# Kernel tuning notes

Hardware: AMD Instinct MI355X
Metric: run time of the kernel (lower is better)

Reference implementation:

```python
import jax, jax.numpy as jnp
import numpy as np
from jax import lax

_W = 0.8           # DVTV chroma weight (init kwarg w)
_ALPHA = 0.02      # forward default alpha
_EPS = 1e-8
_SQ3 = 3.0 ** 0.5; _SQ2 = 2.0 ** 0.5; _SQ6 = 6.0 ** 0.5
# orthonormal color decorrelation (luminance + 2 chroma)
_CMAT = np.array([[1/_SQ3, 1/_SQ3, 1/_SQ3],
                  [1/_SQ2, -1/_SQ2, 0.0],
                  [1/_SQ6, 1/_SQ6, -2/_SQ6]], dtype=np.float32)


def conv_csc(a, B):
    # a: (mb,P,C,M,N), B: (P,C,k,k) -> (mb,C,M,N): x_c = sum_p a_pc (corr) B_pc, SAME pad
    mb, P, C, M, N = a.shape
    a2 = a.transpose(0, 2, 1, 3, 4).reshape(mb, C * P, M, N)
    W = B.transpose(1, 0, 2, 3)  # (C, P, k, k): out=C, in/group=P
    return lax.conv_general_dilated(a2, W, (1, 1), 'SAME',
        dimension_numbers=('NCHW', 'OIHW', 'NCHW'), feature_group_count=C)


def convT_csc(r, B):
    # adjoint of conv_csc: (mb,C,M,N) -> (mb,P,C,M,N) via flipped-kernel correlation
    P, C, k, _ = B.shape
    mb, _, M, N = r.shape
    W = jnp.flip(B, (-2, -1)).transpose(1, 0, 2, 3).reshape(C * P, 1, k, k)
    o = lax.conv_general_dilated(r, W, (1, 1), 'SAME',
        dimension_numbers=('NCHW', 'OIHW', 'NCHW'), feature_group_count=C)
    return o.reshape(mb, C, P, M, N).transpose(0, 2, 1, 3, 4)


def Cop(x):
    return jnp.einsum('dc,bcmn->bdmn', jnp.asarray(_CMAT), x)


def Ctop(x):
    return jnp.einsum('cd,bcmn->bdmn', jnp.asarray(_CMAT), x)


def Dop(x):
    # forward differences, zero at boundary: (mb,C,M,N) -> (mb,2,C,M,N)
    dv = jnp.pad(x[:, :, 1:, :] - x[:, :, :-1, :], ((0, 0), (0, 0), (0, 1), (0, 0)))
    dh = jnp.pad(x[:, :, :, 1:] - x[:, :, :, :-1], ((0, 0), (0, 0), (0, 0), (0, 1)))
    return jnp.stack([dv, dh], axis=1)


def Dtop(y):
    # adjoint of Dop: (mb,2,C,M,N) -> (mb,C,M,N)
    yv = y[:, 0].at[:, :, -1, :].set(0.0)
    yh = y[:, 1].at[:, :, :, -1].set(0.0)
    dv = jnp.pad(yv[:, :, :-1, :], ((0, 0), (0, 0), (1, 0), (0, 0))) - yv
    dh = jnp.pad(yh[:, :, :, :-1], ((0, 0), (0, 0), (0, 0), (1, 0))) - yh
    return dv + dh


def soft(x, t):
    return jnp.sign(x) * jnp.maximum(jnp.abs(x) - t, 0.0)


def prox_dvtv(v, t, w):
    # group soft-threshold: lum group over grad dims; chroma group over grad dims + chroma channels
    lum, ch = v[:, :, 0:1], v[:, :, 1:]
    nl = jnp.sqrt(jnp.sum(lum * lum, axis=1, keepdims=True))
    nc = jnp.sqrt(jnp.sum(ch * ch, axis=(1, 2), keepdims=True))
    sl = jnp.maximum(0.0, 1.0 - t / jnp.maximum(nl, 1e-12))
    sc = jnp.maximum(0.0, 1.0 - (t * w) / jnp.maximum(nc, 1e-12))
    return jnp.concatenate([lum * sl, ch * sc], axis=2)


def proj_l2ball(v, z, radius):
    d = v - z
    n = jnp.sqrt(jnp.sum(d * d, axis=(1, 2, 3), keepdims=True))
    return z + d * jnp.minimum(1.0, radius / jnp.maximum(n, 1e-12))


def setup_inputs() -> dict:
    key = jax.random.key(0)
    k0, k1, k2, k3 = jax.random.split(key, 4)
    mb, C, M, N = 4, 3, 192, 192
    P, ksz, K = 32, 7, 8
    z = jax.random.uniform(k0, (mb, C, M, N), dtype=jnp.float32)
    mask = (jax.random.uniform(k1, (mb, C, M, N)) < 0.5).astype(jnp.float32)
    a0 = 0.01 * jax.random.normal(k2, (mb, P, C, M, N), dtype=jnp.float32)
    B = 0.01 * jax.random.normal(k3, (P, C, ksz, ksz), dtype=jnp.float32)
    # operator norm of B (max singular value of the per-channel filter banks, via FFT)
    Bn = np.asarray(B)
    acc = 0.0
    for c in range(C):
        H = np.fft.fft2(Bn[:, c], s=(64, 64))
        acc += float(np.max(np.sum(np.abs(H) ** 2, axis=0)))
    op_norm = float(np.sqrt(acc))
    beta = (1.0 + op_norm) ** 2
    g1 = 2.0 / beta * 0.9
    g3 = (1.0 / (1.0 + 4 * 2 + _W * 4 * 2)) * (1.0 / g1 - beta / 2.0)
    lam = jnp.full((K,), 5e-4, dtype=jnp.float32)
    return {
        'z': z, 'mask': mask, 'a0': a0, 'B': B,
        'lam1': lam, 'lam2': lam,
        'gam1': jnp.full((K,), g1, dtype=jnp.float32),
        'gam2': jnp.full((K,), g1, dtype=jnp.float32),
        'gam3': jnp.full((K,), g3, dtype=jnp.float32),
    }


def reference(z, mask, a0, B, lam1, lam2, gam1, gam2, gam3):
    mb, C, M, N = z.shape
    K = gam1.shape[0]
    radius = _ALPHA * float(np.sqrt(C * M * N))
    x_bef = z
    a_bef = a0
    y1_bef = jnp.zeros((mb, 2, C, M, N), dtype=z.dtype)
    y2_bef = jnp.zeros((mb, C, M, N), dtype=z.dtype)
    x_aft = x_bef
    for k in range(K):
        r = x_bef - conv_csc(a_bef, B)                     # shared residual
        x = x_bef - gam1[k] * (r + Ctop(Dtop(y1_bef)) + mask * y2_bef)
        x_aft = jnp.clip(x, 0.0, 1.0)                      # ProxBoxConstraint
        a = a_bef + gam2[k] * convT_csc(r, B)
        a_aft = soft(a, gam2[k] * lam1[k])                 # ProxL1
        v = 2.0 * x_aft - x_bef
        y1 = y1_bef + gam3[k] * Dop(Cop(v))
        y1_aft = y1 - gam3[k] * prox_dvtv(y1 / (gam3[k] + _EPS), lam2[k] / (gam3[k] + _EPS), _W)
        y2 = y2_bef + gam3[k] * (mask * v)
        y2_aft = y2 - gam3[k] * proj_l2ball(y2 / (gam3[k] + _EPS), z, radius)
        x_bef, a_bef, y1_bef, y2_bef = x_aft, a_aft, y1_aft, y2_aft
    return x_aft
```

## Files before the change

### kernel.cpp

```cpp
#include <hip/hip_runtime.h>

#define MB 4
#define CC 3
#define MM 192
#define NN 192
#define PP 32
#define KITER 8
#define MN (MM*NN)
#define CMN (CC*MN)
#define IMG (MB*CMN)
#define ASZ (MB*PP*CMN)

#define PSPLIT 16
#define PCHUNK (PP/PSPLIT)

#define PSPLIT_A 4
#define PCHUNK_A (PP/PSPLIT_A)

#define S3 0.57735026918962576f
#define S2 0.70710678118654752f
#define S6 0.40824829046386302f
#define W_CH 0.8f
#define EPSV 1e-8f
#define RADIUS 6.6510751010644885f

#define TD 64
#define HALO 3
#define HROWS 70
#define HCB 18
#define HS2 76
#define NF4 (HROWS*HCB)

#define TDIM 32
#define HT 38
#define HS 40
#define HTT (HT*HT)

__device__ __forceinline__ float softf(float x, float t) {
    float m = fabsf(x) - t;
    return m > 0.f ? copysignf(m, x) : 0.f;
}

__global__ __launch_bounds__(256) void k_conv_part(
    const float* __restrict__ a, const float* __restrict__ Bw,
    float* __restrict__ part)
{
    const int bc = blockIdx.z % (MB*CC);
    const int s  = blockIdx.z / (MB*CC);
    const int b = bc / CC, c = bc % CC;
    const int m0 = blockIdx.y * TD, n0 = blockIdx.x * TD;
    __shared__ float sT[HROWS * HS2];
    const int tc = threadIdx.x & 15;
    const int tr = threadIdx.x >> 4;
    const int p0 = s * PCHUNK;
    const int row0 = threadIdx.x / HCB;
    const int cb0  = threadIdx.x - row0*HCB;

    float4 pf[5];
    {
        const float* ap = a + (size_t)((b*PP + p0)*CC + c) * MN;
        int row = row0, cb = cb0;
        #pragma unroll
        for (int j = 0; j < 5; ++j) {
            const int gm = m0 + row - HALO;
            const int gc = n0 + cb*4 - 4;
            float4 v = {0.f,0.f,0.f,0.f};
            if (row < HROWS && (unsigned)gm < MM && (unsigned)gc <= (NN-4))
                v = *(const float4*)&ap[gm*NN + gc];
            pf[j] = v;
            cb += 4; row += 14; if (cb >= HCB) { cb -= HCB; row += 1; }
        }
    }
    float acc[4][4];
    #pragma unroll
    for (int r = 0; r < 4; ++r)
        #pragma unroll
        for (int j = 0; j < 4; ++j) acc[r][j] = 0.f;

    #pragma unroll 1
    for (int pp = 0; pp < PCHUNK; ++pp) {
        __syncthreads();
        {
            int row = row0, cb = cb0;
            #pragma unroll
            for (int j = 0; j < 5; ++j) {
                if (row < HROWS) *(float4*)&sT[row*HS2 + cb*4] = pf[j];
                cb += 4; row += 14; if (cb >= HCB) { cb -= HCB; row += 1; }
            }
        }
        __syncthreads();
        if (pp + 1 < PCHUNK) {
            const float* ap = a + (size_t)((b*PP + p0 + pp + 1)*CC + c) * MN;
            int row = row0, cb = cb0;
            #pragma unroll
            for (int j = 0; j < 5; ++j) {
                const int gm = m0 + row - HALO;
                const int gc = n0 + cb*4 - 4;
                float4 v = {0.f,0.f,0.f,0.f};
                if (row < HROWS && (unsigned)gm < MM && (unsigned)gc <= (NN-4))
                    v = *(const float4*)&ap[gm*NN + gc];
                pf[j] = v;
                cb += 4; row += 14; if (cb >= HCB) { cb -= HCB; row += 1; }
            }
        }
        const float* bp = Bw + ((p0 + pp)*CC + c) * 49;
        #pragma unroll
        for (int ir = 0; ir < 10; ++ir) {
            const int base = (tr*4 + ir)*HS2 + tc*4;
            const float4 q0 = *(const float4*)&sT[base];
            const float4 q1 = *(const float4*)&sT[base + 4];
            const float4 q2 = *(const float4*)&sT[base + 8];
            const float fl[12] = {q0.x,q0.y,q0.z,q0.w,q1.x,q1.y,q1.z,q1.w,
                                  q2.x,q2.y,q2.z,q2.w};
            #pragma unroll
            for (int r = 0; r < 4; ++r) {
                const int du = ir - r;
                if (du >= 0 && du <= 6) {
                    #pragma unroll
                    for (int v = 0; v < 7; ++v) {
                        const float bv = bp[du*7 + v];
                        #pragma unroll
                        for (int j = 0; j < 4; ++j) acc[r][j] += fl[v+j+1] * bv;
                    }
                }
            }
        }
    }
    #pragma unroll
    for (int r = 0; r < 4; ++r) {
        const int idx = (b*CC + c)*MN + (m0 + tr*4 + r)*NN + n0 + tc*4;
        float4 o; o.x = acc[r][0]; o.y = acc[r][1]; o.z = acc[r][2]; o.w = acc[r][3];
        *(float4*)&part[(size_t)s*IMG + idx] = o;
    }
}

__global__ __launch_bounds__(256) void k_a_update(
    const float* __restrict__ a_in, const float* __restrict__ rr,
    const float* __restrict__ Bw, float* __restrict__ a_out,
    const float* __restrict__ gam2, const float* __restrict__ lam1, int k)
{
    const int bc = blockIdx.z % (MB*CC);
    const int s  = blockIdx.z / (MB*CC);
    const int b = bc / CC, c = bc % CC;
    const int m0 = blockIdx.y * TDIM, n0 = blockIdx.x * TDIM;
    const float g2  = gam2[k];
    const float thr = g2 * lam1[k];
    __shared__ float sT[HT * HS];
    const float* rp = rr + (b*CC + c)*MN;
    for (int i = threadIdx.x; i < HTT; i += 256) {
        const int im = i / HT, in = i - im*HT;
        const int gm = m0 + im - 3, gn = n0 + in - 3;
        float v = 0.f;
        if ((unsigned)gm < MM && (unsigned)gn < NN) v = rp[gm*NN + gn];
        sT[im*HS + in] = v;
    }
    __syncthreads();
    const int row = threadIdx.x >> 3;
    const int tg  = threadIdx.x & 7;
    const int gm = m0 + row;
    const int gn = n0 + tg*4;
    const int p0 = s * PCHUNK_A;
    #pragma unroll 1
    for (int pp = 0; pp < PCHUNK_A; ++pp) {
        const int p = p0 + pp;
        const float* bp = Bw + (p*CC + c) * 49;
        float acc[4] = {0.f, 0.f, 0.f, 0.f};
        #pragma unroll
        for (int u = 0; u < 7; ++u) {
            const int base = (row + 6 - u)*HS + tg*4;
            const float4 q0 = *(const float4*)&sT[base];
            const float4 q1 = *(const float4*)&sT[base + 4];
            const float2 q2 = *(const float2*)&sT[base + 8];
            const float rv[10] = {q0.x,q0.y,q0.z,q0.w,q1.x,q1.y,q1.z,q1.w,q2.x,q2.y};
            #pragma unroll
            for (int v = 0; v < 7; ++v) {
                const float bv = bp[u*7 + v];
                acc[0] += rv[6-v] * bv;
                acc[1] += rv[7-v] * bv;
                acc[2] += rv[8-v] * bv;
                acc[3] += rv[9-v] * bv;
            }
        }
        const size_t idx = (size_t)((b*PP + p)*CC + c)*MN + gm*NN + gn;
        const float4 av = *(const float4*)&a_in[idx];
        float4 o;
        o.x = softf(av.x + g2*acc[0], thr);
        o.y = softf(av.y + g2*acc[1], thr);
        o.z = softf(av.z + g2*acc[2], thr);
        o.w = softf(av.w + g2*acc[3], thr);
        *(float4*)&a_out[idx] = o;
    }
}

__global__ __launch_bounds__(256) void k_x_update(
    const float* __restrict__ xbef, const float* __restrict__ part,
    float* __restrict__ rb,
    const float* __restrict__ y1, float* __restrict__ y2,
    const float* __restrict__ mask, const float* __restrict__ z,
    const float* __restrict__ gam1, const float* __restrict__ gam3, int k,
    float* __restrict__ xaft, float* __restrict__ sums)
{
    const int i = blockIdx.x*256 + threadIdx.x;
    const int b = i / CMN;
    const int rem = i - b*CMN;
    const int c = rem / MN;
    const int mn = rem - c*MN;
    const int m = mn / NN, n = mn - m*NN;
    const float g1 = gam1[k];
    const float g3 = gam3[k];
    const float inv3 = 1.f / (g3 + EPSV);
    float g3p = 0.f, invp = 0.f, scale_prev = 0.f;
    if (k > 0) {
        g3p  = gam3[k-1];
        invp = 1.f / (g3p + EPSV);
        const float nrm = sqrtf(sums[(k-1)*64 + b*16]);
        scale_prev = fminf(1.f, RADIUS / fmaxf(nrm, 1e-12f));
    }
    float dt[3];
    #pragma unroll
    for (int e = 0; e < 3; ++e) {
        const float* yv = y1 + ((size_t)(b*2 + 0)*CC + e)*MN;
        const float* yh = y1 + ((size_t)(b*2 + 1)*CC + e)*MN;
        float dv = (m > 0 ? yv[mn - NN] : 0.f) - (m < MM-1 ? yv[mn] : 0.f);
        float dh = (n > 0 ? yh[mn - 1]  : 0.f) - (n < NN-1 ? yh[mn] : 0.f);
        dt[e] = dv + dh;
    }
    const float ct0 = S3*dt[0] + S2*dt[1] + S6*dt[2];
    const float ct1 = S3*dt[0] - S2*dt[1] + S6*dt[2];
    const float ct2 = S3*dt[0]            - 2.f*S6*dt[2];
    const float ctc = (c == 0) ? ct0 : (c == 1) ? ct1 : ct2;
    const bool last = (k == KITER-1);

    float conv = 0.f;
    #pragma unroll
    for (int ss = 0; ss < PSPLIT; ++ss) conv += part[(size_t)ss*IMG + i];
    const float xb = xbef[i];
    const float r = xb - conv;
    const float zi = z[i];
    const float mk = mask[i];
    float y2b = 0.f;
    if (k > 0) {
        const float yr = y2[i];
        const float d = yr*invp - zi;
        y2b = yr - g3p*(zi + d*scale_prev);
    }
    float x = xb - g1*(r + ctc + mk*y2b);
    x = fminf(fmaxf(x, 0.f), 1.f);
    xaft[i] = x;
    float dsq = 0.f;
    if (!last) {
        rb[i] = r;
        const float v  = 2.f*x - xb;
        const float yn = y2b + g3*(mk*v);
        y2[i] = yn;
        const float d2 = yn*inv3 - zi;
        dsq = d2*d2;
    }
    if (!last) {
        #pragma unroll
        for (int off = 32; off > 0; off >>= 1) dsq += __shfl_down(dsq, off, 64);
        __shared__ float red[4];
        if ((threadIdx.x & 63) == 0) red[threadIdx.x >> 6] = dsq;
        __syncthreads();
        if (threadIdx.x == 0) {
            const int bb = blockIdx.x / (CMN/256);
            atomicAdd(&sums[k*64 + bb*16], red[0] + red[1] + red[2] + red[3]);
        }
    }
}

__global__ __launch_bounds__(256) void k_y1_update(
    float* __restrict__ y1, const float* __restrict__ xaft,
    const float* __restrict__ xbef,
    const float* __restrict__ gam3, const float* __restrict__ lam2, int k)
{
    const int i = blockIdx.x*256 + threadIdx.x;
    if (i >= MB*MN) return;
    const int b = i / MN, mn = i - b*MN;
    const int m = mn / NN, n = mn - m*NN;
    const float g3  = gam3[k];
    const float inv = 1.f / (g3 + EPSV);
    const float t   = lam2[k] * inv;
    const bool hasD = (m < MM-1), hasR = (n < NN-1);
    float vc[3], vd[3], vr[3];
    #pragma unroll
    for (int c = 0; c < 3; ++c) {
        const int idx = (b*CC + c)*MN + mn;
        vc[c] = 2.f*xaft[idx] - xbef[idx];
        vd[c] = hasD ? (2.f*xaft[idx+NN] - xbef[idx+NN]) : 0.f;
        vr[c] = hasR ? (2.f*xaft[idx+1]  - xbef[idx+1])  : 0.f;
    }
    const float cc0 = S3*(vc[0]+vc[1]+vc[2]);
    const float cc1 = S2*(vc[0]-vc[1]);
    const float cc2 = S6*(vc[0]+vc[1]) - 2.f*S6*vc[2];
    const float cd0 = S3*(vd[0]+vd[1]+vd[2]);
    const float cd1 = S2*(vd[0]-vd[1]);
    const float cd2 = S6*(vd[0]+vd[1]) - 2.f*S6*vd[2];
    const float cr0 = S3*(vr[0]+vr[1]+vr[2]);
    const float cr1 = S2*(vr[0]-vr[1]);
    const float cr2 = S6*(vr[0]+vr[1]) - 2.f*S6*vr[2];
    const float dv[3] = { hasD ? cd0-cc0 : 0.f, hasD ? cd1-cc1 : 0.f, hasD ? cd2-cc2 : 0.f };
    const float dh[3] = { hasR ? cr0-cc0 : 0.f, hasR ? cr1-cc1 : 0.f, hasR ? cr2-cc2 : 0.f };
    float yn[2][3], vv[2][3];
    #pragma unroll
    for (int e = 0; e < 3; ++e) {
        const int i0 = ((b*2 + 0)*CC + e)*MN + mn;
        const int i1 = ((b*2 + 1)*CC + e)*MN + mn;
        yn[0][e] = y1[i0] + g3*dv[e];
        yn[1][e] = y1[i1] + g3*dh[e];
        vv[0][e] = yn[0][e]*inv;
        vv[1][e] = yn[1][e]*inv;
    }
    const float nl = sqrtf(vv[0][0]*vv[0][0] + vv[1][0]*vv[1][0]);
    const float sl = fmaxf(0.f, 1.f - t / fmaxf(nl, 1e-12f));
    const float nc = sqrtf(vv[0][1]*vv[0][1] + vv[0][2]*vv[0][2]
                         + vv[1][1]*vv[1][1] + vv[1][2]*vv[1][2]);
    const float sc = fmaxf(0.f, 1.f - t*W_CH / fmaxf(nc, 1e-12f));
    #pragma unroll
    for (int e = 0; e < 3; ++e) {
        const float se = (e == 0) ? sl : sc;
        const int i0 = ((b*2 + 0)*CC + e)*MN + mn;
        const int i1 = ((b*2 + 1)*CC + e)*MN + mn;
        y1[i0] = yn[0][e] - g3*(vv[0][e]*se);
        y1[i1] = yn[1][e] - g3*(vv[1][e]*se);
    }
}

extern "C" void kernel_launch(void* const* d_in, const int* in_sizes, int n_in,
                              void* d_out, int out_size, void* d_ws, size_t ws_size,
                              hipStream_t stream) {
    const float* z    = (const float*)d_in[0];
    const float* mask = (const float*)d_in[1];
    const float* a0   = (const float*)d_in[2];
    const float* Bw   = (const float*)d_in[3];
    const float* lam1 = (const float*)d_in[4];
    const float* lam2 = (const float*)d_in[5];
    const float* gam1 = (const float*)d_in[6];
    const float* gam2 = (const float*)d_in[7];
    const float* gam3 = (const float*)d_in[8];
    float* out = (float*)d_out;

    float* ws = (float*)d_ws;
    float* xA   = ws; ws += IMG;
    float* xB   = ws; ws += IMG;
    float* y1   = ws; ws += 2*IMG;
    float* y2   = ws; ws += IMG;
    float* rb   = ws; ws += IMG;
    float* part = ws; ws += PSPLIT*IMG;
    float* sums = ws; ws += KITER*64;
    const size_t base_need = (size_t)((6 + PSPLIT)*IMG + KITER*64) * sizeof(float);
    float* a_ws;
    if (ws_size >= base_need + (size_t)ASZ * sizeof(float)) {
        a_ws = ws;
    } else {
        a_ws = (float*)d_in[2];
    }

    hipMemsetAsync(y1, 0, sizeof(float)*2*IMG, stream);
    hipMemsetAsync(sums, 0, sizeof(float)*KITER*64, stream);

    dim3 gconv(NN/TD, MM/TD, MB*CC*PSPLIT);
    dim3 ga(NN/TDIM, MM/TDIM, MB*CC*PSPLIT_A);
    const int ew_blocks  = (MB*MN) / 256;
    const int img_blocks = IMG / 256;

    const float* xbef = z;
    float* xaft = xA;
    const float* acur = a0;
    for (int k = 0; k < KITER; ++k) {
        k_conv_part<<<gconv, 256, 0, stream>>>(acur, Bw, part);
        float* xt = (k == KITER-1) ? out : xaft;
        k_x_update<<<img_blocks, 256, 0, stream>>>(xbef, part, rb, y1, y2, mask, z,
                                                   gam1, gam3, k, xt, sums);
        if (k < KITER-1) {
            k_a_update<<<ga, 256, 0, stream>>>(acur, rb, Bw, a_ws, gam2, lam1, k);
            k_y1_update<<<ew_blocks, 256, 0, stream>>>(y1, xt, xbef, gam3, lam2, k);
            acur = a_ws;
            xbef = xt;
            xaft = (xt == xA) ? xB : xA;
        }
    }
    (void)in_sizes; (void)n_in; (void)out_size;
}
```

Before: 730.3 us.

## Fuse sparse-code update with next iteration's forward convolution via shared-memory tile

The a-update kernel now computes the updated, soft-thresholded coefficients over a 38x38 tile with a 3-pixel halo and keeps it in shared memory. It then applies the forward convolution for the next iteration directly from that tile and writes per-split partial sums. This removes the separate forward-convolution kernel for every iteration after the first, along with its full re-read of the large coefficient tensor. In exchange, the halo region's update is recomputed redundantly by neighbouring tiles, the partial-sum split count changes, and coefficients are ping-ponged through the caller's a0 input buffer, which is overwritten.

```diff
diff --git a/kernel.cpp b/kernel.cpp
--- a/kernel.cpp
+++ b/kernel.cpp
@@ -14,8 +14,8 @@
 #define PSPLIT 16
 #define PCHUNK (PP/PSPLIT)
 
-#define PSPLIT_A 4
-#define PCHUNK_A (PP/PSPLIT_A)
+#define PSPLIT_F 4
+#define PCHUNK_F (PP/PSPLIT_F)
 
 #define S3 0.57735026918962576f
 #define S2 0.70710678118654752f
@@ -29,12 +29,10 @@
 #define HROWS 70
 #define HCB 18
 #define HS2 76
-#define NF4 (HROWS*HCB)
 
 #define TDIM 32
-#define HT 38
-#define HS 40
-#define HTT (HT*HT)
+#define SRS 48
+#define SAS 40
 
 __device__ __forceinline__ float softf(float x, float t) {
     float m = fabsf(x) - t;
@@ -134,9 +132,10 @@
     }
 }
 
-__global__ __launch_bounds__(256) void k_a_update(
-    const float* __restrict__ a_in, const float* __restrict__ rr,
+__global__ __launch_bounds__(256) void k_aconv(
+    const float* __restrict__ a_in, const float* __restrict__ rb,
     const float* __restrict__ Bw, float* __restrict__ a_out,
+    float* __restrict__ part,
     const float* __restrict__ gam2, const float* __restrict__ lam1, int k)
 {
     const int bc = blockIdx.z % (MB*CC);
@@ -145,55 +144,101 @@
     const int m0 = blockIdx.y * TDIM, n0 = blockIdx.x * TDIM;
     const float g2  = gam2[k];
     const float thr = g2 * lam1[k];
-    __shared__ float sT[HT * HS];
-    const float* rp = rr + (b*CC + c)*MN;
-    for (int i = threadIdx.x; i < HTT; i += 256) {
-        const int im = i / HT, in = i - im*HT;
-        const int gm = m0 + im - 3, gn = n0 + in - 3;
-        float v = 0.f;
-        if ((unsigned)gm < MM && (unsigned)gn < NN) v = rp[gm*NN + gn];
-        sT[im*HS + in] = v;
+    __shared__ float sR[44 * SRS];
+    __shared__ float sA[38 * SAS];
+
+    {
+        const float* rp = rb + (size_t)(b*CC + c) * MN;
+        #pragma unroll
+        for (int pass = 0; pass < 3; ++pass) {
+            const int f = threadIdx.x + pass*256;
+            if (f < 44*12) {
+                const int rrow = f / 12, rcb = f - rrow*12;
+                const int grow = m0 + rrow - 6;
+                const int gc4  = n0 - 8 + rcb*4;
+                float4 v = {0.f,0.f,0.f,0.f};
+                if ((unsigned)grow < MM && (unsigned)gc4 <= (NN-4))
+                    v = *(const float4*)&rp[grow*NN + gc4];
+                *(float4*)&sR[rrow*SRS + rcb*4] = v;
+            }
+        }
     }
     __syncthreads();
+
     const int row = threadIdx.x >> 3;
     const int tg  = threadIdx.x & 7;
-    const int gm = m0 + row;
-    const int gn = n0 + tg*4;
-    const int p0 = s * PCHUNK_A;
+    const int p0 = s * PCHUNK_F;
+    float accc[4] = {0.f, 0.f, 0.f, 0.f};
+
     #pragma unroll 1
-    for (int pp = 0; pp < PCHUNK_A; ++pp) {
+    for (int pp = 0; pp < PCHUNK_F; ++pp) {
         const int p = p0 + pp;
+        const size_t pbase = (size_t)((b*PP + p)*CC + c) * MN;
         const float* bp = Bw + (p*CC + c) * 49;
-        float acc[4] = {0.f, 0.f, 0.f, 0.f};
+
+        #pragma unroll
+        for (int pass = 0; pass < 2; ++pass) {
+            const int t = threadIdx.x + pass*256;
+            if (t < 380) {
+                const int ar  = t / 10;
+                const int acb = t - ar*10;
+                float acc[4] = {0.f, 0.f, 0.f, 0.f};
+                #pragma unroll
+                for (int u = 0; u < 7; ++u) {
+                    const float* srow = &sR[(ar + 6 - u)*SRS + acb*4];
+                    const float4 q0 = *(const float4*)&srow[0];
+                    const float4 q1 = *(const float4*)&srow[4];
+                    const float4 q2 = *(const float4*)&srow[8];
+                    const float fl[12] = {q0.x,q0.y,q0.z,q0.w,q1.x,q1.y,q1.z,q1.w,
+                                          q2.x,q2.y,q2.z,q2.w};
+                    #pragma unroll
+                    for (int v = 0; v < 7; ++v) {
+                        const float bv = bp[u*7 + v];
+                        #pragma unroll
+                        for (int j = 0; j < 4; ++j) acc[j] += fl[7 - v + j] * bv;
+                    }
+                }
+                const int gma = m0 + ar - 3;
+                const int gc4 = n0 - 4 + acb*4;
+                const bool ok = ((unsigned)gma < MM) && ((unsigned)gc4 <= (NN-4));
+                float4 av = {0.f,0.f,0.f,0.f};
+                if (ok) av = *(const float4*)&a_in[pbase + gma*NN + gc4];
+                float4 an;
+                an.x = ok ? softf(av.x + g2*acc[0], thr) : 0.f;
+                an.y = ok ? softf(av.y + g2*acc[1], thr) : 0.f;
+                an.z = ok ? softf(av.z + g2*acc[2], thr) : 0.f;
+                an.w = ok ? softf(av.w + g2*acc[3], thr) : 0.f;
+                *(float4*)&sA[ar*SAS + acb*4] = an;
+                if (ar >= 3 && ar <= 34 && acb >= 1 && acb <= 8)
+                    *(float4*)&a_out[pbase + gma*NN + gc4] = an;
+            }
+        }
+        __syncthreads();
+
         #pragma unroll
         for (int u = 0; u < 7; ++u) {
-            const int base = (row + 6 - u)*HS + tg*4;
-            const float4 q0 = *(const float4*)&sT[base];
-            const float4 q1 = *(const float4*)&sT[base + 4];
-            const float2 q2 = *(const float2*)&sT[base + 8];
-            const float rv[10] = {q0.x,q0.y,q0.z,q0.w,q1.x,q1.y,q1.z,q1.w,q2.x,q2.y};
+            const float* srow = &sA[(row + u)*SAS + tg*4];
+            const float4 q0 = *(const float4*)&srow[0];
+            const float4 q1 = *(const float4*)&srow[4];
+            const float4 q2 = *(const float4*)&srow[8];
+            const float fl[12] = {q0.x,q0.y,q0.z,q0.w,q1.x,q1.y,q1.z,q1.w,
+                                  q2.x,q2.y,q2.z,q2.w};
             #pragma unroll
             for (int v = 0; v < 7; ++v) {
                 const float bv = bp[u*7 + v];
-                acc[0] += rv[6-v] * bv;
-                acc[1] += rv[7-v] * bv;
-                acc[2] += rv[8-v] * bv;
-                acc[3] += rv[9-v] * bv;
-            }
-        }
-        const size_t idx = (size_t)((b*PP + p)*CC + c)*MN + gm*NN + gn;
-        const float4 av = *(const float4*)&a_in[idx];
-        float4 o;
-        o.x = softf(av.x + g2*acc[0], thr);
-        o.y = softf(av.y + g2*acc[1], thr);
-        o.z = softf(av.z + g2*acc[2], thr);
-        o.w = softf(av.w + g2*acc[3], thr);
-        *(float4*)&a_out[idx] = o;
-    }
+                #pragma unroll
+                for (int j = 0; j < 4; ++j) accc[j] += fl[1 + v + j] * bv;
+            }
+        }
+        __syncthreads();
+    }
+    const int idx = (b*CC + c)*MN + (m0 + row)*NN + n0 + tg*4;
+    float4 o; o.x = accc[0]; o.y = accc[1]; o.z = accc[2]; o.w = accc[3];
+    *(float4*)&part[(size_t)s*IMG + idx] = o;
 }
 
 __global__ __launch_bounds__(256) void k_x_update(
-    const float* __restrict__ xbef, const float* __restrict__ part,
+    const float* __restrict__ xbef, const float* __restrict__ part, int nsplit,
     float* __restrict__ rb,
     const float* __restrict__ y1, float* __restrict__ y2,
     const float* __restrict__ mask, const float* __restrict__ z,
@@ -232,8 +277,8 @@
     const bool last = (k == KITER-1);
 
     float conv = 0.f;
-    #pragma unroll
-    for (int ss = 0; ss < PSPLIT; ++ss) conv += part[(size_t)ss*IMG + i];
+    #pragma unroll 4
+    for (int ss = 0; ss < nsplit; ++ss) conv += part[(size_t)ss*IMG + i];
     const float xb = xbef[i];
     const float r = xb - conv;
     const float zi = z[i];
@@ -331,7 +376,7 @@
                               hipStream_t stream) {
     const float* z    = (const float*)d_in[0];
     const float* mask = (const float*)d_in[1];
-    const float* a0   = (const float*)d_in[2];
+    float*       a0   = (float*)d_in[2];
     const float* Bw   = (const float*)d_in[3];
     const float* lam1 = (const float*)d_in[4];
     const float* lam2 = (const float*)d_in[5];
@@ -349,33 +394,38 @@
     float* part = ws; ws += PSPLIT*IMG;
     float* sums = ws; ws += KITER*64;
     const size_t base_need = (size_t)((6 + PSPLIT)*IMG + KITER*64) * sizeof(float);
-    float* a_ws;
+    float* aA;
     if (ws_size >= base_need + (size_t)ASZ * sizeof(float)) {
-        a_ws = ws;
+        aA = ws;
     } else {
-        a_ws = (float*)d_in[2];
-    }
+        aA = a0;
+    }
+    float* aB = a0;
 
     hipMemsetAsync(y1, 0, sizeof(float)*2*IMG, stream);
     hipMemsetAsync(sums, 0, sizeof(float)*KITER*64, stream);
 
     dim3 gconv(NN/TD, MM/TD, MB*CC*PSPLIT);
-    dim3 ga(NN/TDIM, MM/TDIM, MB*CC*PSPLIT_A);
+    dim3 gf(NN/TDIM, MM/TDIM, MB*CC*PSPLIT_F);
     const int ew_blocks  = (MB*MN) / 256;
     const int img_blocks = IMG / 256;
 
     const float* xbef = z;
     float* xaft = xA;
     const float* acur = a0;
+    float* anext = aA;
     for (int k = 0; k < KITER; ++k) {
-        k_conv_part<<<gconv, 256, 0, stream>>>(acur, Bw, part);
+        if (k == 0)
+            k_conv_part<<<gconv, 256, 0, stream>>>(acur, Bw, part);
         float* xt = (k == KITER-1) ? out : xaft;
-        k_x_update<<<img_blocks, 256, 0, stream>>>(xbef, part, rb, y1, y2, mask, z,
+        k_x_update<<<img_blocks, 256, 0, stream>>>(xbef, part, (k == 0) ? PSPLIT : PSPLIT_F,
+                                                   rb, y1, y2, mask, z,
                                                    gam1, gam3, k, xt, sums);
         if (k < KITER-1) {
-            k_a_update<<<ga, 256, 0, stream>>>(acur, rb, Bw, a_ws, gam2, lam1, k);
+            k_aconv<<<gf, 256, 0, stream>>>(acur, rb, Bw, anext, part, gam2, lam1, k);
             k_y1_update<<<ew_blocks, 256, 0, stream>>>(y1, xt, xbef, gam3, lam2, k);
-            acur = a_ws;
+            acur = anext;
+            anext = (anext == aA) ? aB : aA;
             xbef = xt;
             xaft = (xt == xA) ? xB : xA;
         }
```

Result: slower. 1.532 ms (+109.8%).

## Drop shared-memory staging in conv kernels and read halos directly from global

Applied to the files above, without the earlier changes.

Both convolution kernels stop staging halo tiles in LDS and instead load float4 rows straight from global memory, relying on L1/L2 for reuse. The forward conv drops to 3 output rows per thread, uses 48x64 tiles and halves the P-split, which shrinks the partial-sum buffer the x-update reduces. The adjoint conv flips its loop order to reuse each residual row across all filters in its chunk, keeping 8x4 accumulators. The cost is more redundant global/cache traffic for overlapping halos and higher register pressure in exchange for removing syncs and LDS round trips.

```diff
diff --git a/kernel.cpp b/kernel.cpp
--- a/kernel.cpp
+++ b/kernel.cpp
@@ -11,9 +11,8 @@
 #define IMG (MB*CMN)
 #define ASZ (MB*PP*CMN)
 
-#define PSPLIT 16
-#define PCHUNK (PP/PSPLIT)
-
+#define PSPLIT_C 8
+#define PCHUNK_C (PP/PSPLIT_C)
 #define PSPLIT_A 4
 #define PCHUNK_A (PP/PSPLIT_A)
 
@@ -24,101 +23,55 @@
 #define EPSV 1e-8f
 #define RADIUS 6.6510751010644885f
 
-#define TD 64
-#define HALO 3
-#define HROWS 70
-#define HCB 18
-#define HS2 76
-#define NF4 (HROWS*HCB)
-
+#define TCW 64
+#define TCH 48
 #define TDIM 32
-#define HT 38
-#define HS 40
-#define HTT (HT*HT)
 
 __device__ __forceinline__ float softf(float x, float t) {
     float m = fabsf(x) - t;
     return m > 0.f ? copysignf(m, x) : 0.f;
 }
 
-__global__ __launch_bounds__(256) void k_conv_part(
+__global__ __launch_bounds__(256) void k_conv(
     const float* __restrict__ a, const float* __restrict__ Bw,
     float* __restrict__ part)
 {
     const int bc = blockIdx.z % (MB*CC);
     const int s  = blockIdx.z / (MB*CC);
     const int b = bc / CC, c = bc % CC;
-    const int m0 = blockIdx.y * TD, n0 = blockIdx.x * TD;
-    __shared__ float sT[HROWS * HS2];
+    const int m0 = blockIdx.y * TCH, n0 = blockIdx.x * TCW;
     const int tc = threadIdx.x & 15;
     const int tr = threadIdx.x >> 4;
-    const int p0 = s * PCHUNK;
-    const int row0 = threadIdx.x / HCB;
-    const int cb0  = threadIdx.x - row0*HCB;
-
-    float4 pf[5];
-    {
-        const float* ap = a + (size_t)((b*PP + p0)*CC + c) * MN;
-        int row = row0, cb = cb0;
-        #pragma unroll
-        for (int j = 0; j < 5; ++j) {
-            const int gm = m0 + row - HALO;
-            const int gc = n0 + cb*4 - 4;
-            float4 v = {0.f,0.f,0.f,0.f};
-            if (row < HROWS && (unsigned)gm < MM && (unsigned)gc <= (NN-4))
-                v = *(const float4*)&ap[gm*NN + gc];
-            pf[j] = v;
-            cb += 4; row += 14; if (cb >= HCB) { cb -= HCB; row += 1; }
-        }
-    }
-    float acc[4][4];
-    #pragma unroll
-    for (int r = 0; r < 4; ++r)
-        #pragma unroll
-        for (int j = 0; j < 4; ++j) acc[r][j] = 0.f;
+    const int gc = n0 + tc*4 - 4;
+    const bool pc0 = (unsigned)gc       <= (NN-4);
+    const bool pc1 = (unsigned)(gc + 4) <= (NN-4);
+    const bool pc2 = (unsigned)(gc + 8) <= (NN-4);
+    const int rbase = m0 + tr*3 - 3;
+    const int p0 = s * PCHUNK_C;
+    float acc[3][4] = {{0.f}};
 
     #pragma unroll 1
-    for (int pp = 0; pp < PCHUNK; ++pp) {
-        __syncthreads();
-        {
-            int row = row0, cb = cb0;
-            #pragma unroll
-            for (int j = 0; j < 5; ++j) {
-                if (row < HROWS) *(float4*)&sT[row*HS2 + cb*4] = pf[j];
-                cb += 4; row += 14; if (cb >= HCB) { cb -= HCB; row += 1; }
-            }
-        }
-        __syncthreads();
-        if (pp + 1 < PCHUNK) {
-            const float* ap = a + (size_t)((b*PP + p0 + pp + 1)*CC + c) * MN;
-            int row = row0, cb = cb0;
-            #pragma unroll
-            for (int j = 0; j < 5; ++j) {
-                const int gm = m0 + row - HALO;
-                const int gc = n0 + cb*4 - 4;
-                float4 v = {0.f,0.f,0.f,0.f};
-                if (row < HROWS && (unsigned)gm < MM && (unsigned)gc <= (NN-4))
-                    v = *(const float4*)&ap[gm*NN + gc];
-                pf[j] = v;
-                cb += 4; row += 14; if (cb >= HCB) { cb -= HCB; row += 1; }
-            }
-        }
+    for (int pp = 0; pp < PCHUNK_C; ++pp) {
+        const float* ap = a + (size_t)((b*PP + p0 + pp)*CC + c) * MN;
         const float* bp = Bw + ((p0 + pp)*CC + c) * 49;
         #pragma unroll
-        for (int ir = 0; ir < 10; ++ir) {
-            const int base = (tr*4 + ir)*HS2 + tc*4;
-            const float4 q0 = *(const float4*)&sT[base];
-            const float4 q1 = *(const float4*)&sT[base + 4];
-            const float4 q2 = *(const float4*)&sT[base + 8];
+        for (int u = 0; u < 9; ++u) {
+            const int gm = rbase + u;
+            const bool pr = (unsigned)gm < MM;
+            const float* rowp = ap + gm*NN;
+            const float4 z4 = make_float4(0.f,0.f,0.f,0.f);
+            const float4 q0 = (pr && pc0) ? *(const float4*)(rowp + gc)     : z4;
+            const float4 q1 = (pr && pc1) ? *(const float4*)(rowp + gc + 4) : z4;
+            const float4 q2 = (pr && pc2) ? *(const float4*)(rowp + gc + 8) : z4;
             const float fl[12] = {q0.x,q0.y,q0.z,q0.w,q1.x,q1.y,q1.z,q1.w,
                                   q2.x,q2.y,q2.z,q2.w};
             #pragma unroll
-            for (int r = 0; r < 4; ++r) {
-                const int du = ir - r;
-                if (du >= 0 && du <= 6) {
+            for (int r = 0; r < 3; ++r) {
+                const int d = u - r;
+                if (d >= 0 && d <= 6) {
                     #pragma unroll
                     for (int v = 0; v < 7; ++v) {
-                        const float bv = bp[du*7 + v];
+                        const float bv = bp[d*7 + v];
                         #pragma unroll
                         for (int j = 0; j < 4; ++j) acc[r][j] += fl[v+j+1] * bv;
                     }
@@ -127,15 +80,15 @@
         }
     }
     #pragma unroll
-    for (int r = 0; r < 4; ++r) {
-        const int idx = (b*CC + c)*MN + (m0 + tr*4 + r)*NN + n0 + tc*4;
+    for (int r = 0; r < 3; ++r) {
+        const int idx = (b*CC + c)*MN + (m0 + tr*3 + r)*NN + n0 + tc*4;
         float4 o; o.x = acc[r][0]; o.y = acc[r][1]; o.z = acc[r][2]; o.w = acc[r][3];
         *(float4*)&part[(size_t)s*IMG + idx] = o;
     }
 }
 
 __global__ __launch_bounds__(256) void k_a_update(
-    const float* __restrict__ a_in, const float* __restrict__ rr,
+    const float* __restrict__ a_in, const float* __restrict__ rb,
     const float* __restrict__ Bw, float* __restrict__ a_out,
     const float* __restrict__ gam2, const float* __restrict__ lam1, int k)
 {
@@ -145,49 +98,50 @@
     const int m0 = blockIdx.y * TDIM, n0 = blockIdx.x * TDIM;
     const float g2  = gam2[k];
     const float thr = g2 * lam1[k];
-    __shared__ float sT[HT * HS];
-    const float* rp = rr + (b*CC + c)*MN;
-    for (int i = threadIdx.x; i < HTT; i += 256) {
-        const int im = i / HT, in = i - im*HT;
-        const int gm = m0 + im - 3, gn = n0 + in - 3;
-        float v = 0.f;
-        if ((unsigned)gm < MM && (unsigned)gn < NN) v = rp[gm*NN + gn];
-        sT[im*HS + in] = v;
-    }
-    __syncthreads();
     const int row = threadIdx.x >> 3;
     const int tg  = threadIdx.x & 7;
     const int gm = m0 + row;
     const int gn = n0 + tg*4;
+    const int gc = gn - 4;
+    const bool pc0 = (unsigned)gc       <= (NN-4);
+    const bool pc1 = (unsigned)(gc + 4) <= (NN-4);
+    const bool pc2 = (unsigned)(gc + 8) <= (NN-4);
     const int p0 = s * PCHUNK_A;
-    #pragma unroll 1
-    for (int pp = 0; pp < PCHUNK_A; ++pp) {
-        const int p = p0 + pp;
-        const float* bp = Bw + (p*CC + c) * 49;
-        float acc[4] = {0.f, 0.f, 0.f, 0.f};
+    const float* rbp = rb + (size_t)(b*CC + c) * MN;
+    const float* Bc  = Bw + c * 49;
+
+    float acc[PCHUNK_A][4] = {{0.f}};
+    #pragma unroll
+    for (int u = 0; u < 7; ++u) {
+        const int gmr = gm + 3 - u;
+        const bool pr = (unsigned)gmr < MM;
+        const float* rowp = rbp + gmr*NN;
+        const float4 z4 = make_float4(0.f,0.f,0.f,0.f);
+        const float4 q0 = (pr && pc0) ? *(const float4*)(rowp + gc)     : z4;
+        const float4 q1 = (pr && pc1) ? *(const float4*)(rowp + gc + 4) : z4;
+        const float4 q2 = (pr && pc2) ? *(const float4*)(rowp + gc + 8) : z4;
+        const float fl[12] = {q0.x,q0.y,q0.z,q0.w,q1.x,q1.y,q1.z,q1.w,
+                              q2.x,q2.y,q2.z,q2.w};
         #pragma unroll
-        for (int u = 0; u < 7; ++u) {
-            const int base = (row + 6 - u)*HS + tg*4;
-            const float4 q0 = *(const float4*)&sT[base];
-            const float4 q1 = *(const float4*)&sT[base + 4];
-            const float2 q2 = *(const float2*)&sT[base + 8];
-            const float rv[10] = {q0.x,q0.y,q0.z,q0.w,q1.x,q1.y,q1.z,q1.w,q2.x,q2.y};
+        for (int pp = 0; pp < PCHUNK_A; ++pp) {
+            const float* bp = Bc + (p0 + pp)*(CC*49) + u*7;
             #pragma unroll
             for (int v = 0; v < 7; ++v) {
-                const float bv = bp[u*7 + v];
-                acc[0] += rv[6-v] * bv;
-                acc[1] += rv[7-v] * bv;
-                acc[2] += rv[8-v] * bv;
-                acc[3] += rv[9-v] * bv;
+                const float bv = bp[v];
+                #pragma unroll
+                for (int j = 0; j < 4; ++j) acc[pp][j] += fl[7 - v + j] * bv;
             }
         }
-        const size_t idx = (size_t)((b*PP + p)*CC + c)*MN + gm*NN + gn;
+    }
+    #pragma unroll
+    for (int pp = 0; pp < PCHUNK_A; ++pp) {
+        const size_t idx = (size_t)((b*PP + p0 + pp)*CC + c)*MN + gm*NN + gn;
         const float4 av = *(const float4*)&a_in[idx];
         float4 o;
-        o.x = softf(av.x + g2*acc[0], thr);
-        o.y = softf(av.y + g2*acc[1], thr);
-        o.z = softf(av.z + g2*acc[2], thr);
-        o.w = softf(av.w + g2*acc[3], thr);
+        o.x = softf(av.x + g2*acc[pp][0], thr);
+        o.y = softf(av.y + g2*acc[pp][1], thr);
+        o.z = softf(av.z + g2*acc[pp][2], thr);
+        o.w = softf(av.w + g2*acc[pp][3], thr);
         *(float4*)&a_out[idx] = o;
     }
 }
@@ -233,7 +187,7 @@
 
     float conv = 0.f;
     #pragma unroll
-    for (int ss = 0; ss < PSPLIT; ++ss) conv += part[(size_t)ss*IMG + i];
+    for (int ss = 0; ss < PSPLIT_C; ++ss) conv += part[(size_t)ss*IMG + i];
     const float xb = xbef[i];
     const float r = xb - conv;
     const float zi = z[i];
@@ -346,9 +300,9 @@
     float* y1   = ws; ws += 2*IMG;
     float* y2   = ws; ws += IMG;
     float* rb   = ws; ws += IMG;
-    float* part = ws; ws += PSPLIT*IMG;
+    float* part = ws; ws += PSPLIT_C*IMG;
     float* sums = ws; ws += KITER*64;
-    const size_t base_need = (size_t)((6 + PSPLIT)*IMG + KITER*64) * sizeof(float);
+    const size_t base_need = (size_t)((6 + PSPLIT_C)*IMG + KITER*64) * sizeof(float);
     float* a_ws;
     if (ws_size >= base_need + (size_t)ASZ * sizeof(float)) {
         a_ws = ws;
@@ -359,7 +313,7 @@
     hipMemsetAsync(y1, 0, sizeof(float)*2*IMG, stream);
     hipMemsetAsync(sums, 0, sizeof(float)*KITER*64, stream);
 
-    dim3 gconv(NN/TD, MM/TD, MB*CC*PSPLIT);
+    dim3 gconv(NN/TCW, MM/TCH, MB*CC*PSPLIT_C);
     dim3 ga(NN/TDIM, MM/TDIM, MB*CC*PSPLIT_A);
     const int ew_blocks  = (MB*MN) / 256;
     const int img_blocks = IMG / 256;
@@ -368,7 +322,7 @@
     float* xaft = xA;
     const float* acur = a0;
     for (int k = 0; k < KITER; ++k) {
-        k_conv_part<<<gconv, 256, 0, stream>>>(acur, Bw, part);
+        k_conv<<<gconv, 256, 0, stream>>>(acur, Bw, part);
         float* xt = (k == KITER-1) ? out : xaft;
         k_x_update<<<img_blocks, 256, 0, stream>>>(xbef, part, rb, y1, y2, mask, z,
                                                    gam1, gam3, k, xt, sums);
```

New measurement: 1.430 ms. +95.9%, slower.
